# Optimization experiments

Hardware: AMD Instinct MI355X
Metric: run time of the kernel (lower is better)

Reference implementation:

```python
import jax, jax.numpy as jnp
import numpy as np

B, L, C = 16, 720, 862
RANK, K = 8, 7
EPS = 1e-5


def setup_inputs() -> dict:
    key = jax.random.key(0)
    ks = jax.random.split(key, 7)
    x = jax.random.normal(ks[0], (B, L, C), dtype=jnp.float32)
    # Conv1d(1 -> rank, k): PyTorch init ~ U(-s, s), s = 1/sqrt(in_ch*k)
    s_up = 1.0 / np.sqrt(1 * K)
    Wup = jax.random.uniform(ks[1], (RANK, 1, K), jnp.float32, -s_up, s_up)
    bup = jax.random.uniform(ks[2], (RANK,), jnp.float32, -s_up, s_up)
    # Conv1d(rank -> 1, 1)
    s_dn = 1.0 / np.sqrt(RANK * 1)
    Wdown = jax.random.uniform(ks[3], (1, RANK, 1), jnp.float32, -s_dn, s_dn)
    bdown = jax.random.uniform(ks[4], (1,), jnp.float32, -s_dn, s_dn)
    gamma = jnp.ones((C,), jnp.float32)
    beta = jnp.zeros((C,), jnp.float32)
    return {"x": x, "Wup": Wup, "bup": bup, "Wdown": Wdown,
            "bdown": bdown, "gamma": gamma, "beta": beta}


def reference(x, Wup, bup, Wdown, bdown, gamma, beta):
    b, l, c = x.shape
    h = x.reshape(b * l, 1, c)  # (N, 1, C): conv along variable dim
    pad = K // 2
    h = jax.lax.conv_general_dilated(
        h, Wup, window_strides=(1,), padding=[(pad, pad)],
        dimension_numbers=("NCH", "OIH", "NCH"))
    h = h + bup[None, :, None]                      # (N, rank, C)
    h = jax.nn.gelu(h, approximate=False)           # torch F.gelu default = erf
    # 1x1 conv down: contraction over rank channels
    h = jnp.einsum("nrc,r->nc", h, Wdown[0, :, 0]) + bdown[0]  # (N, C)
    y = x + h.reshape(b, l, c)                      # residual
    # LayerNorm over last dim (n_vars), eps=1e-5
    mu = jnp.mean(y, axis=-1, keepdims=True)
    var = jnp.mean(jnp.square(y - mu), axis=-1, keepdims=True)
    y = (y - mu) * jax.lax.rsqrt(var + EPS)
    return y * gamma + beta
```

## Files before the change

kernel.cpp:

```cpp
#include <hip/hip_runtime.h>
#include <math.h>

#define CDIM   862
#define NRANK  8
#define KW     7
#define ROWS_PER_BLOCK 4
#define THREADS (ROWS_PER_BLOCK * 64)
#define LN_EPS 1e-5f
#define NTILE  27
#define XH_LEN 880
#define XY_LEN 866

typedef __attribute__((ext_vector_type(8)))  short bf16x8;
typedef __attribute__((ext_vector_type(16))) float f32x16;

static __device__ __forceinline__ unsigned rne_bf16(float f) {
    const unsigned u = __float_as_uint(f);
    return (u + 0x7FFFu + ((u >> 16) & 1u)) >> 16;
}

__global__ __launch_bounds__(THREADS) void cvmc_kernel(
    const float* __restrict__ x,
    const float* __restrict__ Wup,
    const float* __restrict__ bup,
    const float* __restrict__ Wdown,
    const float* __restrict__ bdown,
    const float* __restrict__ gamma,
    const float* __restrict__ beta,
    float* __restrict__ out)
{
    const int lane = threadIdx.x & 63;
    const int wv   = threadIdx.x >> 6;
    const int row  = blockIdx.x * ROWS_PER_BLOCK + wv;

    __shared__ short sxh[ROWS_PER_BLOCK][XH_LEN];
    __shared__ float sxy[ROWS_PER_BLOCK][XY_LEN];

    const int hh    = lane >> 5;
    const int rbase = 4 * hh;
    float bu4[4], wd4[4];
#pragma unroll
    for (int q = 0; q < 4; ++q) {
        bu4[q] = bup[rbase + q];
        wd4[q] = Wdown[rbase + q];
    }
    const float bdv = bdown[0];

    bf16x8 afrag;
    {
        const int r = lane & 31;
        const bool arow = (hh == 0) && (r < NRANK);
#pragma unroll
        for (int j = 0; j < 8; ++j) {
            float wvv = 0.0f;
            if (arow && j < KW) wvv = Wup[r * KW + j];
            afrag[j] = (short)(rne_bf16(wvv) & 0xFFFFu);
        }
    }

    {
        const float2* __restrict__ xr2 =
            reinterpret_cast<const float2*>(x + (size_t)row * CDIM);
        unsigned* xhW = reinterpret_cast<unsigned*>(&sxh[wv][0]);
#pragma unroll
        for (int qq = 0; qq < 7; ++qq) {
            const int i = lane + 64 * qq;
            if (i < CDIM / 2) {
                float2 v = xr2[i];
                *reinterpret_cast<float2*>(&sxy[wv][2 * i]) = v;
                xhW[2 + i] = rne_bf16(v.x) | (rne_bf16(v.y) << 16);
            }
        }
        if (lane < 2)       xhW[lane] = 0u;
        else if (lane < 9)  xhW[431 + lane] = 0u;
        else if (lane < 13) sxy[wv][862 + (lane - 9)] = 0.0f;
    }

    const float C1 = -0.0713548162f;
    const float C0 = -1.5957691216f;

    f32x16 zero16;
#pragma unroll
    for (int i = 0; i < 16; ++i) zero16[i] = 0.0f;

    float sum = 0.0f, sumsq = 0.0f;

    const unsigned* xhD = reinterpret_cast<const unsigned*>(&sxh[wv][0]);
    const int l31 = lane & 31;

    for (int t = 0; t < NTILE; ++t) {
        const int c  = 32 * t + l31;
        const int ws = c + 1;

        const unsigned* pw = xhD + (ws >> 1);
        const unsigned sh = (unsigned)(ws & 1) * 16u;
        const unsigned q0 = pw[0], q1 = pw[1], q2 = pw[2], q3 = pw[3], q4 = pw[4];
        union { unsigned u[4]; bf16x8 v; } bfr;
        bfr.u[0] = __builtin_amdgcn_alignbit(q1, q0, sh);
        bfr.u[1] = __builtin_amdgcn_alignbit(q2, q1, sh);
        bfr.u[2] = __builtin_amdgcn_alignbit(q3, q2, sh);
        bfr.u[3] = __builtin_amdgcn_alignbit(q4, q3, sh);

        f32x16 d = __builtin_amdgcn_mfma_f32_32x32x16_bf16(afrag, bfr.v, zero16, 0, 0, 0);

        float t0 = d[0] + bu4[0];
        float t1 = d[1] + bu4[1];
        float t2 = d[2] + bu4[2];
        float t3 = d[3] + bu4[3];

        const float z0 = t0 * fmaf(t0 * t0, C1, C0);
        const float z1 = t1 * fmaf(t1 * t1, C1, C0);
        const float z2 = t2 * fmaf(t2 * t2, C1, C0);
        const float z3 = t3 * fmaf(t3 * t3, C1, C0);
        const float u0 = 1.0f + __expf(z0);
        const float u1 = 1.0f + __expf(z1);
        const float u2 = 1.0f + __expf(z2);
        const float u3 = 1.0f + __expf(z3);
        const float r01 = __builtin_amdgcn_rcpf(u0 * u1);
        const float r23 = __builtin_amdgcn_rcpf(u2 * u3);
        float n0 = (wd4[0] * t0) * u1; n0 = fmaf(wd4[1] * t1, u0, n0);
        float n1 = (wd4[2] * t2) * u3; n1 = fmaf(wd4[3] * t3, u2, n1);
        float p  = n0 * r01;
        p = fmaf(n1, r23, p);

        const float psum = p + __shfl_xor(p, 32, 64);

        const float xv = sxy[wv][c];
        float y = xv + bdv + psum;
        if (c >= CDIM) y = 0.0f;
        if (lane < 32) sxy[wv][c] = y;
        sum += y;
        sumsq = fmaf(y, y, sumsq);
    }

#pragma unroll
    for (int off = 1; off < 64; off <<= 1) {
        sum   += __shfl_xor(sum, off, 64);
        sumsq += __shfl_xor(sumsq, off, 64);
    }

    const float inv  = 0.5f / (float)CDIM;
    const float mu   = sum * inv;
    const float var  = fmaf(sumsq, inv, -mu * mu);
    const float rstd = rsqrtf(var + LN_EPS);

    float2* __restrict__ yr2 = reinterpret_cast<float2*>(out + (size_t)row * CDIM);
    const float2* __restrict__ g2 = reinterpret_cast<const float2*>(gamma);
    const float2* __restrict__ b2 = reinterpret_cast<const float2*>(beta);
#pragma unroll
    for (int qq = 0; qq < 7; ++qq) {
        const int i = lane + 64 * qq;
        if (i < CDIM / 2) {
            const float2 yv = *reinterpret_cast<const float2*>(&sxy[wv][2 * i]);
            const float2 gv = g2[i];
            const float2 bv = b2[i];
            float2 o;
            o.x = fmaf((yv.x - mu) * rstd, gv.x, bv.x);
            o.y = fmaf((yv.y - mu) * rstd, gv.y, bv.y);
            yr2[i] = o;
        }
    }
}

extern "C" void kernel_launch(void* const* d_in, const int* in_sizes, int n_in,
                              void* d_out, int out_size, void* d_ws, size_t ws_size,
                              hipStream_t stream) {
    const float* x     = (const float*)d_in[0];
    const float* Wup   = (const float*)d_in[1];
    const float* bup   = (const float*)d_in[2];
    const float* Wdown = (const float*)d_in[3];
    const float* bdown = (const float*)d_in[4];
    const float* gamma = (const float*)d_in[5];
    const float* beta  = (const float*)d_in[6];
    float* out = (float*)d_out;

    const int nrows = out_size / CDIM;
    const int nblk  = nrows / ROWS_PER_BLOCK;
    cvmc_kernel<<<nblk, THREADS, 0, stream>>>(x, Wup, bup, Wdown, bdown,
                                              gamma, beta, out);
}
```

Baseline: 44.27 us.

## Pack two column tiles per MFMA using both row halves of the A fragment

```diff
diff --git a/kernel.cpp b/kernel.cpp
--- a/kernel.cpp
+++ b/kernel.cpp
@@ -7,7 +7,7 @@
 #define ROWS_PER_BLOCK 4
 #define THREADS (ROWS_PER_BLOCK * 64)
 #define LN_EPS 1e-5f
-#define NTILE  27
+#define NPAIRT 13
 #define XH_LEN 880
 #define XY_LEN 866
 
@@ -37,6 +37,7 @@
     __shared__ float sxy[ROWS_PER_BLOCK][XY_LEN];
 
     const int hh    = lane >> 5;
+    const int l31   = lane & 31;
     const int rbase = 4 * hh;
     float bu4[4], wd4[4];
 #pragma unroll
@@ -48,15 +49,20 @@
 
     bf16x8 afrag;
     {
-        const int r = lane & 31;
-        const bool arow = (hh == 0) && (r < NRANK);
+        const bool use = (hh == 0) ? (l31 < NRANK) : (l31 >= 8 && l31 < 8 + NRANK);
+        const int  rr  = (hh == 0) ? l31 : (l31 - 8);
 #pragma unroll
         for (int j = 0; j < 8; ++j) {
-            float wvv = 0.0f;
-            if (arow && j < KW) wvv = Wup[r * KW + j];
+            float wvv = (use && j < KW) ? Wup[rr * KW + j] : 0.0f;
             afrag[j] = (short)(rne_bf16(wvv) & 0xFFFFu);
         }
     }
+
+    f32x16 cin;
+#pragma unroll
+    for (int i = 0; i < 16; ++i) cin[i] = 0.0f;
+#pragma unroll
+    for (int q = 0; q < 8; ++q) cin[q] = bu4[q & 3];
 
     {
         const float2* __restrict__ xr2 =
@@ -79,35 +85,9 @@
     const float C1 = -0.0713548162f;
     const float C0 = -1.5957691216f;
 
-    f32x16 zero16;
-#pragma unroll
-    for (int i = 0; i < 16; ++i) zero16[i] = 0.0f;
-
-    float sum = 0.0f, sumsq = 0.0f;
-
     const unsigned* xhD = reinterpret_cast<const unsigned*>(&sxh[wv][0]);
-    const int l31 = lane & 31;
-
-    for (int t = 0; t < NTILE; ++t) {
-        const int c  = 32 * t + l31;
-        const int ws = c + 1;
-
-        const unsigned* pw = xhD + (ws >> 1);
-        const unsigned sh = (unsigned)(ws & 1) * 16u;
-        const unsigned q0 = pw[0], q1 = pw[1], q2 = pw[2], q3 = pw[3], q4 = pw[4];
-        union { unsigned u[4]; bf16x8 v; } bfr;
-        bfr.u[0] = __builtin_amdgcn_alignbit(q1, q0, sh);
-        bfr.u[1] = __builtin_amdgcn_alignbit(q2, q1, sh);
-        bfr.u[2] = __builtin_amdgcn_alignbit(q3, q2, sh);
-        bfr.u[3] = __builtin_amdgcn_alignbit(q4, q3, sh);
-
-        f32x16 d = __builtin_amdgcn_mfma_f32_32x32x16_bf16(afrag, bfr.v, zero16, 0, 0, 0);
-
-        float t0 = d[0] + bu4[0];
-        float t1 = d[1] + bu4[1];
-        float t2 = d[2] + bu4[2];
-        float t3 = d[3] + bu4[3];
-
+
+    auto dp4 = [&](float t0, float t1, float t2, float t3) -> float {
         const float z0 = t0 * fmaf(t0 * t0, C1, C0);
         const float z1 = t1 * fmaf(t1 * t1, C1, C0);
         const float z2 = t2 * fmaf(t2 * t2, C1, C0);
@@ -121,16 +101,61 @@
         float n0 = (wd4[0] * t0) * u1; n0 = fmaf(wd4[1] * t1, u0, n0);
         float n1 = (wd4[2] * t2) * u3; n1 = fmaf(wd4[3] * t3, u2, n1);
         float p  = n0 * r01;
-        p = fmaf(n1, r23, p);
-
-        const float psum = p + __shfl_xor(p, 32, 64);
-
-        const float xv = sxy[wv][c];
-        float y = xv + bdv + psum;
-        if (c >= CDIM) y = 0.0f;
-        if (lane < 32) sxy[wv][c] = y;
+        return fmaf(n1, r23, p);
+    };
+
+    float sum = 0.0f, sumsq = 0.0f;
+
+    for (int s = 0; s < NPAIRT; ++s) {
+        const int cw = 64 * s + lane;
+        const int ws = cw + 1;
+
+        const unsigned* pw = xhD + (ws >> 1);
+        const unsigned sh = (unsigned)(ws & 1) * 16u;
+        const unsigned q0 = pw[0], q1 = pw[1], q2 = pw[2], q3 = pw[3], q4 = pw[4];
+        union { unsigned u[4]; bf16x8 v; } bfr;
+        bfr.u[0] = __builtin_amdgcn_alignbit(q1, q0, sh);
+        bfr.u[1] = __builtin_amdgcn_alignbit(q2, q1, sh);
+        bfr.u[2] = __builtin_amdgcn_alignbit(q3, q2, sh);
+        bfr.u[3] = __builtin_amdgcn_alignbit(q4, q3, sh);
+
+        f32x16 d = __builtin_amdgcn_mfma_f32_32x32x16_bf16(afrag, bfr.v, cin, 0, 0, 0);
+
+        const float pA = dp4(d[0], d[1], d[2], d[3]);
+        const float pB = dp4(d[4], d[5], d[6], d[7]);
+        const float hA = pA + __shfl_xor(pA, 32, 64);
+        const float hB = pB + __shfl_xor(pB, 32, 64);
+        const float h  = (hh == 0) ? hA : hB;
+
+        const float xv = sxy[wv][cw];
+        const float y  = xv + bdv + h;
+        sxy[wv][cw] = y;
         sum += y;
         sumsq = fmaf(y, y, sumsq);
+    }
+
+    {
+        const int c  = 832 + l31;
+        const int ws = c + 1;
+        const unsigned* pw = xhD + (ws >> 1);
+        const unsigned sh = (unsigned)(ws & 1) * 16u;
+        const unsigned q0 = pw[0], q1 = pw[1], q2 = pw[2], q3 = pw[3], q4 = pw[4];
+        union { unsigned u[4]; bf16x8 v; } bfr;
+        bfr.u[0] = __builtin_amdgcn_alignbit(q1, q0, sh);
+        bfr.u[1] = __builtin_amdgcn_alignbit(q2, q1, sh);
+        bfr.u[2] = __builtin_amdgcn_alignbit(q3, q2, sh);
+        bfr.u[3] = __builtin_amdgcn_alignbit(q4, q3, sh);
+
+        f32x16 d = __builtin_amdgcn_mfma_f32_32x32x16_bf16(afrag, bfr.v, cin, 0, 0, 0);
+
+        const float p = dp4(d[0], d[1], d[2], d[3]);
+        const float psum = p + __shfl_xor(p, 32, 64);
+        const float y = sxy[wv][c] + bdv + psum;
+        if (hh == 0 && c < CDIM) {
+            sxy[wv][c] = y;
+            sum += y;
+            sumsq = fmaf(y, y, sumsq);
+        }
     }
 
 #pragma unroll
@@ -139,7 +164,7 @@
         sumsq += __shfl_xor(sumsq, off, 64);
     }
 
-    const float inv  = 0.5f / (float)CDIM;
+    const float inv  = 1.0f / (float)CDIM;
     const float mu   = sum * inv;
     const float var  = fmaf(sumsq, inv, -mu * mu);
     const float rstd = rsqrtf(var + LN_EPS);
```

Measured after the change: 38.34 us. 13.4% less time.
